# Optimization experiments

Measured on AMD Instinct MI355X. Metric: run time of the kernel, lower is better.

Reference implementation:

```python
import jax, jax.numpy as jnp
import numpy as np

B, V = 64, 128000
N_TEMP, PIECES = 1, 8
THR_MIN, THR_MAX = -3.0, 3.0
TEMP_CLAMP_MIN = 0.0001


def setup_inputs() -> dict:
    key = jax.random.key(0)
    k1, k2 = jax.random.split(key)
    logits = jax.random.normal(k1, (B, V), dtype=jnp.float32)
    # learned params (mode='absolute', init_temp='random', init_thresholds='linspace')
    temperature = jax.random.uniform(k2, (N_TEMP, PIECES), dtype=jnp.float32)  # torch.rand init
    thresholds = jnp.tile(jnp.linspace(THR_MIN, THR_MAX, PIECES - 1, dtype=jnp.float32)[None, :],
                          (N_TEMP, 1))  # (n_temp, P-1)
    return {"logits": logits, "temperature": temperature, "thresholds": thresholds}


def reference(logits, temperature, thresholds):
    # TemperatureScaler.forward with mode='absolute', pieces>1, i=0, temp_mask=False.
    # Matches apply_temperature_with_grad math (the path taken when params require grad).
    T = jnp.clip(temperature[0], TEMP_CLAMP_MIN, None)      # (P,) clamped temperatures
    thr = jnp.sort(thresholds[0])                           # (P-1,) sorted thresholds
    # bin id per logit: searchsorted(thr, logit), side='left' (torch default)
    bin_ids = jnp.searchsorted(thr, logits)                 # (B, V) int in [0, P-1]
    # continuity constants: c = cumsum(diff(pad(thr, left 0)) * T[:-1])
    diffs = jnp.diff(jnp.pad(thr, (1, 0)))                  # (P-1,)
    c = jnp.cumsum(diffs * T[:-1])                          # (P-1,)
    # per-bin affine: bin 0 -> T0 * x ; bin b>=1 -> T[b]*(x - thr[b-1]) + c[b-1]
    thr_pad = jnp.pad(thr, (1, 0))                          # (P,), thr_pad[0] = 0
    c_pad = jnp.pad(c, (1, 0))                              # (P,), c_pad[0] = 0
    return T[bin_ids] * (logits - thr_pad[bin_ids]) + c_pad[bin_ids]
```

## Files before the change

### kernel.cpp

```cpp
#include <hip/hip_runtime.h>


#define PIECES 8
#define NTHR (PIECES - 1)
#define TEMP_CLAMP_MIN 1e-4f

__global__ __launch_bounds__(256) void temp_scale_kernel(
    const float4* __restrict__ x4,
    float4* __restrict__ out4,
    const float* __restrict__ temperature,
    const float* __restrict__ thresholds,
    int n4, int n_tail, const float* __restrict__ x_tail_base,
    float* __restrict__ out_tail_base)
{
    __shared__ float sT[PIECES];
    __shared__ float sTP[PIECES];
    __shared__ float sCP[PIECES];

    if (threadIdx.x == 0) {
        float T[PIECES], thr[NTHR];
        #pragma unroll
        for (int j = 0; j < PIECES; ++j) T[j] = fmaxf(temperature[j], TEMP_CLAMP_MIN);
        #pragma unroll
        for (int j = 0; j < NTHR; ++j) thr[j] = thresholds[j];
        for (int i = 1; i < NTHR; ++i) {
            float key = thr[i];
            int j = i - 1;
            while (j >= 0 && thr[j] > key) { thr[j + 1] = thr[j]; --j; }
            thr[j + 1] = key;
        }
        float prev = 0.f, acc = 0.f;
        sTP[0] = 0.f; sCP[0] = 0.f;
        for (int k = 0; k < NTHR; ++k) {
            acc += (thr[k] - prev) * T[k];
            prev = thr[k];
            sTP[k + 1] = thr[k];
            sCP[k + 1] = acc;
        }
        #pragma unroll
        for (int j = 0; j < PIECES; ++j) sT[j] = T[j];
    }
    __syncthreads();

    float T[PIECES], tp[PIECES], cp[PIECES];
    #pragma unroll
    for (int j = 0; j < PIECES; ++j) { T[j] = sT[j]; tp[j] = sTP[j]; cp[j] = sCP[j]; }

    const int stride = gridDim.x * blockDim.x;
    int i = blockIdx.x * blockDim.x + threadIdx.x;

    for (; i < n4; i += stride) {
        float4 v = x4[i];
        float xs[4] = {v.x, v.y, v.z, v.w};
        float r[4];
        #pragma unroll
        for (int e = 0; e < 4; ++e) {
            float x = xs[e];
            float t = T[0], a = 0.f, c = 0.f;
            #pragma unroll
            for (int j = 1; j < PIECES; ++j) {
                bool gt = x > tp[j];
                t = gt ? T[j] : t;
                a = gt ? tp[j] : a;
                c = gt ? cp[j] : c;
            }
            r[e] = fmaf(t, x - a, c);
        }
        out4[i] = make_float4(r[0], r[1], r[2], r[3]);
    }

    int gid = blockIdx.x * blockDim.x + threadIdx.x;
    if (gid < n_tail) {
        float x = x_tail_base[gid];
        float t = T[0], a = 0.f, c = 0.f;
        #pragma unroll
        for (int j = 1; j < PIECES; ++j) {
            bool gt = x > tp[j];
            t = gt ? T[j] : t;
            a = gt ? tp[j] : a;
            c = gt ? cp[j] : c;
        }
        out_tail_base[gid] = fmaf(t, x - a, c);
    }
}

extern "C" void kernel_launch(void* const* d_in, const int* in_sizes, int n_in,
                              void* d_out, int out_size, void* d_ws, size_t ws_size,
                              hipStream_t stream) {
    const float* logits      = (const float*)d_in[0];
    const float* temperature = (const float*)d_in[1];
    const float* thresholds  = (const float*)d_in[2];
    float* out = (float*)d_out;

    const int n = in_sizes[0];
    const int n4 = n / 4;
    const int n_tail = n - n4 * 4;

    const int block = 256;
    int grid = (n4 + block - 1) / block;
    if (grid < 1) grid = 1;

    temp_scale_kernel<<<grid, block, 0, stream>>>(
        (const float4*)logits, (float4*)out, temperature, thresholds,
        n4, n_tail, logits + (size_t)n4 * 4, out + (size_t)n4 * 4);
}
```

Before: 88.51 us.

## Compute params per thread, cap grid, and unroll grid-stride loop by four

Each thread now builds the sorted thresholds and continuity constants in registers using a branchless sorting network, which drops the shared-memory staging and the block barrier. The grid is capped at 2000 blocks, and the grid-stride loop issues four float4 loads before computing, to raise memory-level parallelism per thread. In exchange every thread repeats the small parameter setup, and the fixed grid cap may underfill or overfill the device.

After: 86.89 us. About the same (-1.8%).

```diff
diff --git a/kernel.cpp b/kernel.cpp
--- a/kernel.cpp
+++ b/kernel.cpp
@@ -4,6 +4,57 @@
 #define PIECES 8
 #define NTHR (PIECES - 1)
 #define TEMP_CLAMP_MIN 1e-4f
+
+struct Params {
+    float T[PIECES];
+    float tp[PIECES];
+    float cp[PIECES];
+};
+
+__device__ __forceinline__ Params make_params(const float* __restrict__ temperature,
+                                              const float* __restrict__ thresholds) {
+    Params P;
+    float thr[NTHR];
+    #pragma unroll
+    for (int j = 0; j < PIECES; ++j) P.T[j] = fmaxf(temperature[j], TEMP_CLAMP_MIN);
+    #pragma unroll
+    for (int j = 0; j < NTHR; ++j) thr[j] = thresholds[j];
+    #pragma unroll
+    for (int i = 0; i < NTHR - 1; ++i) {
+        #pragma unroll
+        for (int j = 0; j < NTHR - 1 - i; ++j) {
+            float lo = fminf(thr[j], thr[j + 1]);
+            float hi = fmaxf(thr[j], thr[j + 1]);
+            thr[j] = lo; thr[j + 1] = hi;
+        }
+    }
+    float prev = 0.f, acc = 0.f;
+    P.tp[0] = 0.f; P.cp[0] = 0.f;
+    #pragma unroll
+    for (int k = 0; k < NTHR; ++k) {
+        acc += (thr[k] - prev) * P.T[k];
+        prev = thr[k];
+        P.tp[k + 1] = thr[k];
+        P.cp[k + 1] = acc;
+    }
+    return P;
+}
+
+__device__ __forceinline__ float apply1(const Params& P, float x) {
+    float t = P.T[0], a = 0.f, c = 0.f;
+    #pragma unroll
+    for (int j = 1; j < PIECES; ++j) {
+        bool gt = x > P.tp[j];
+        t = gt ? P.T[j] : t;
+        a = gt ? P.tp[j] : a;
+        c = gt ? P.cp[j] : c;
+    }
+    return fmaf(t, x - a, c);
+}
+
+__device__ __forceinline__ float4 apply4(const Params& P, float4 v) {
+    return make_float4(apply1(P, v.x), apply1(P, v.y), apply1(P, v.z), apply1(P, v.w));
+}
 
 __global__ __launch_bounds__(256) void temp_scale_kernel(
     const float4* __restrict__ x4,
@@ -13,75 +64,25 @@
     int n4, int n_tail, const float* __restrict__ x_tail_base,
     float* __restrict__ out_tail_base)
 {
-    __shared__ float sT[PIECES];
-    __shared__ float sTP[PIECES];
-    __shared__ float sCP[PIECES];
-
-    if (threadIdx.x == 0) {
-        float T[PIECES], thr[NTHR];
-        #pragma unroll
-        for (int j = 0; j < PIECES; ++j) T[j] = fmaxf(temperature[j], TEMP_CLAMP_MIN);
-        #pragma unroll
-        for (int j = 0; j < NTHR; ++j) thr[j] = thresholds[j];
-        for (int i = 1; i < NTHR; ++i) {
-            float key = thr[i];
-            int j = i - 1;
-            while (j >= 0 && thr[j] > key) { thr[j + 1] = thr[j]; --j; }
-            thr[j + 1] = key;
-        }
-        float prev = 0.f, acc = 0.f;
-        sTP[0] = 0.f; sCP[0] = 0.f;
-        for (int k = 0; k < NTHR; ++k) {
-            acc += (thr[k] - prev) * T[k];
-            prev = thr[k];
-            sTP[k + 1] = thr[k];
-            sCP[k + 1] = acc;
-        }
-        #pragma unroll
-        for (int j = 0; j < PIECES; ++j) sT[j] = T[j];
-    }
-    __syncthreads();
-
-    float T[PIECES], tp[PIECES], cp[PIECES];
-    #pragma unroll
-    for (int j = 0; j < PIECES; ++j) { T[j] = sT[j]; tp[j] = sTP[j]; cp[j] = sCP[j]; }
+    const Params P = make_params(temperature, thresholds);
 
     const int stride = gridDim.x * blockDim.x;
-    int i = blockIdx.x * blockDim.x + threadIdx.x;
+    const int tid = blockIdx.x * blockDim.x + threadIdx.x;
 
-    for (; i < n4; i += stride) {
-        float4 v = x4[i];
-        float xs[4] = {v.x, v.y, v.z, v.w};
-        float r[4];
-        #pragma unroll
-        for (int e = 0; e < 4; ++e) {
-            float x = xs[e];
-            float t = T[0], a = 0.f, c = 0.f;
-            #pragma unroll
-            for (int j = 1; j < PIECES; ++j) {
-                bool gt = x > tp[j];
-                t = gt ? T[j] : t;
-                a = gt ? tp[j] : a;
-                c = gt ? cp[j] : c;
-            }
-            r[e] = fmaf(t, x - a, c);
-        }
-        out4[i] = make_float4(r[0], r[1], r[2], r[3]);
+    int i = tid;
+    for (; i + 3 * stride < n4; i += 4 * stride) {
+        float4 a = x4[i];
+        float4 b = x4[i + stride];
+        float4 c = x4[i + 2 * stride];
+        float4 d = x4[i + 3 * stride];
+        out4[i]              = apply4(P, a);
+        out4[i + stride]     = apply4(P, b);
+        out4[i + 2 * stride] = apply4(P, c);
+        out4[i + 3 * stride] = apply4(P, d);
     }
+    for (; i < n4; i += stride) out4[i] = apply4(P, x4[i]);
 
-    int gid = blockIdx.x * blockDim.x + threadIdx.x;
-    if (gid < n_tail) {
-        float x = x_tail_base[gid];
-        float t = T[0], a = 0.f, c = 0.f;
-        #pragma unroll
-        for (int j = 1; j < PIECES; ++j) {
-            bool gt = x > tp[j];
-            t = gt ? T[j] : t;
-            a = gt ? tp[j] : a;
-            c = gt ? cp[j] : c;
-        }
-        out_tail_base[gid] = fmaf(t, x - a, c);
-    }
+    if (tid < n_tail) out_tail_base[tid] = apply1(P, x_tail_base[tid]);
 }
 
 extern "C" void kernel_launch(void* const* d_in, const int* in_sizes, int n_in,
@@ -97,7 +98,9 @@
     const int n_tail = n - n4 * 4;
 
     const int block = 256;
-    int grid = (n4 + block - 1) / block;
+    int grid = 2000;
+    int need = (n4 + block - 1) / block;
+    if (need < grid) grid = need;
     if (grid < 1) grid = 1;
 
     temp_scale_kernel<<<grid, block, 0, stream>>>(
```
